# Performance work log

Measured on AMD Instinct MI355X. Metric: run time of the kernel, lower is better.

The kernel has to match this reference:

```python
import jax, jax.numpy as jnp
import numpy as np

B, N, D, H = 4, 1024, 1024, 16
DK = D // H
NEG_INF = jnp.finfo(jnp.float32).min


def setup_inputs() -> dict:
    key = jax.random.key(0)
    ks = jax.random.split(key, 6)
    x = jax.random.normal(ks[0], (B, N, D), dtype=jnp.float32)
    # padding mask: True where padded; vary lengths per batch element
    lengths = jnp.array([N, N - 128, N - 256, N - 512], dtype=jnp.int32)
    mask = jnp.arange(N)[None, :] >= lengths[:, None]  # [B, N] bool
    s = (1.0 / np.sqrt(D)).astype(np.float32)  # xavier-ish scale
    Wq = jax.random.normal(ks[1], (D, D), dtype=jnp.float32) * s
    Wk = jax.random.normal(ks[2], (D, D), dtype=jnp.float32) * s
    Wv = jax.random.normal(ks[3], (D, D), dtype=jnp.float32) * s
    Wo = jax.random.normal(ks[4], (D, D), dtype=jnp.float32) * s
    z = jnp.zeros((D,), dtype=jnp.float32)
    return {"x": x, "mask": mask, "Wq": Wq, "bq": z, "Wk": Wk, "bk": z,
            "Wv": Wv, "bv": z, "Wo": Wo, "bo": z}


def reference(x, mask, Wq, bq, Wk, bk, Wv, bv, Wo, bo):
    b, n, d = x.shape
    scale = jnp.asarray(DK, x.dtype) ** -0.5
    # QKV projections (weights stored [out, in] like torch Linear)
    def proj(W, bias):
        y = jnp.einsum('bnd,ed->bne', x, W) + bias
        return y.reshape(b, n, H, DK).transpose(0, 2, 1, 3)  # [B,H,N,Dk]
    q = proj(Wq, bq)
    k = proj(Wk, bk)
    v = proj(Wv, bv)
    energy = jnp.einsum('bhqd,bhkd->bhqk', q, k) * scale  # [B,H,N,N]
    energy = jnp.where(mask[:, None, None, :], NEG_INF, energy)
    weights = jax.nn.softmax(energy, axis=-1)
    attn = jnp.einsum('bhqk,bhkd->bhqd', weights, v)  # [B,H,N,Dk]
    attn = attn.transpose(0, 2, 1, 3).reshape(b, n, d)
    return jnp.einsum('bnd,ed->bne', attn, Wo) + bo
```

## Files before the change

kernel.cpp:

```cpp
#include <hip/hip_runtime.h>

#define DEV __device__ __forceinline__

typedef __attribute__((ext_vector_type(8))) short s16x8;
typedef __attribute__((ext_vector_type(4))) float f32x4;
typedef __attribute__((ext_vector_type(4))) unsigned short u16x4;
typedef __attribute__((ext_vector_type(2))) unsigned int u32x2;

static constexpr int Bb = 4, Nn = 1024, Dd = 1024, Hh = 16, DKk = 64;

DEV unsigned short f2bf(float f) {
    union { float f; unsigned int u; } x; x.f = f;
    unsigned int r = x.u + 0x7FFFu + ((x.u >> 16) & 1u);
    return (unsigned short)(r >> 16);
}

DEV float fexp2(float x) {
#if __has_builtin(__builtin_amdgcn_exp2f)
    return __builtin_amdgcn_exp2f(x);
#else
    return exp2f(x);
#endif
}

DEV void gld16(const void* g, void* l) {
    __builtin_amdgcn_global_load_lds(
        (const __attribute__((address_space(1))) void*)g,
        (__attribute__((address_space(3))) void*)l, 16, 0, 0);
}

__global__ void decode_mask_k(const unsigned int* __restrict__ raw, int* __restrict__ lengths) {
    __shared__ int is_u8;
    const int tid = threadIdx.x;
    if (tid == 0) is_u8 = 0;
    __syncthreads();
    int nz = 0;
    for (int i = tid; i < 1024; i += 256) nz |= (raw[i] != 0u) ? 1 : 0;
    if (nz) is_u8 = 1;
    __syncthreads();
    const int wv = tid >> 6, lane = tid & 63;
    int cnt = 0;
    if (is_u8) {
        const unsigned char* b8 = (const unsigned char*)raw;
        for (int n = lane; n < Nn; n += 64) cnt += (b8[wv * Nn + n] == 0) ? 1 : 0;
    } else {
        for (int n = lane; n < Nn; n += 64) cnt += (raw[wv * Nn + n] == 0u) ? 1 : 0;
    }
#pragma unroll
    for (int off = 32; off; off >>= 1) cnt += __shfl_xor(cnt, off);
    if (lane == 0) lengths[wv] = cnt;
}

__global__ __launch_bounds__(256) void cast_k(const float* __restrict__ x,
                                              const float* __restrict__ Wq,
                                              const float* __restrict__ Wk,
                                              const float* __restrict__ Wv,
                                              const float* __restrict__ Wo,
                                              unsigned short* __restrict__ xb,
                                              unsigned short* __restrict__ Wqb,
                                              unsigned short* __restrict__ Wkb,
                                              unsigned short* __restrict__ Wvb,
                                              unsigned short* __restrict__ Wob) {
    const size_t i = ((size_t)blockIdx.x * 256 + threadIdx.x) * 8;
    const float* src;
    unsigned short* dst;
    size_t off;
    const size_t XE = (size_t)4 * 1024 * 1024, WE = (size_t)1024 * 1024;
    if (i < XE) {
        src = x; dst = xb; off = i;
    } else {
        size_t j = i - XE;
        int w = (int)(j >> 20);
        off = j & (WE - 1);
        src = (w == 0) ? Wq : (w == 1) ? Wk : (w == 2) ? Wv : Wo;
        dst = (w == 0) ? Wqb : (w == 1) ? Wkb : (w == 2) ? Wvb : Wob;
    }
    f32x4 a = *(const f32x4*)(src + off);
    f32x4 b = *(const f32x4*)(src + off + 4);
    s16x8 t;
    t[0] = (short)f2bf(a[0]); t[1] = (short)f2bf(a[1]);
    t[2] = (short)f2bf(a[2]); t[3] = (short)f2bf(a[3]);
    t[4] = (short)f2bf(b[0]); t[5] = (short)f2bf(b[1]);
    t[6] = (short)f2bf(b[2]); t[7] = (short)f2bf(b[3]);
    *(s16x8*)(dst + off) = t;
}

DEV void gemm_kloop(const unsigned short* __restrict__ A,
                    const unsigned short* __restrict__ W,
                    char* lA, char* lB, int bm, int bn,
                    int tid, int kstep0, f32x4 (&acc)[4][4]) {
    const int wv = tid >> 6, lane = tid & 63, g = lane >> 4, lr = lane & 15;
    const int wr = wv >> 1, wc = wv & 1;

    const int rbase = wv * 8 + (lane >> 3);
    const int corig = (lane & 7) ^ (lane >> 3);
    const unsigned short* Asrc = A + (size_t)(bm + rbase) * Dd + corig * 8;
    const unsigned short* Bsrc = W + (size_t)(bn + rbase) * Dd + corig * 8;
    const int ldsb = wv * 1024;
    const int xk = (lr & 7);

    int kstep = kstep0;
    for (int it = 0; it < 16; ++it) {
        const int k0 = kstep * 64;
#pragma unroll
        for (int p = 0; p < 4; ++p) {
            gld16(Asrc + (size_t)(p * 32) * Dd + k0, lA + p * 4096 + ldsb);
            gld16(Bsrc + (size_t)(p * 32) * Dd + k0, lB + p * 4096 + ldsb);
        }
        __syncthreads();
#pragma unroll
        for (int s = 0; s < 2; ++s) {
            s16x8 af[4], bf[4];
#pragma unroll
            for (int m = 0; m < 4; ++m)
                af[m] = *(const s16x8*)(lA + (wr * 64 + m * 16 + lr) * 128 + (((s * 4 + g) ^ xk) << 4));
#pragma unroll
            for (int n = 0; n < 4; ++n)
                bf[n] = *(const s16x8*)(lB + (wc * 64 + n * 16 + lr) * 128 + (((s * 4 + g) ^ xk) << 4));
#pragma unroll
            for (int m = 0; m < 4; ++m)
#pragma unroll
                for (int n = 0; n < 4; ++n)
                    acc[m][n] = __builtin_amdgcn_mfma_f32_16x16x32_bf16(af[m], bf[n], acc[m][n], 0, 0, 0);
        }
        __syncthreads();
        kstep = (kstep + 1) & 15;
    }
}

__global__ __launch_bounds__(256, 4) void gemm_qkv_k(const unsigned short* __restrict__ xb,
                                                     const unsigned short* __restrict__ Wqb,
                                                     const unsigned short* __restrict__ Wkb,
                                                     const unsigned short* __restrict__ Wvb,
                                                     const float* __restrict__ bq,
                                                     const float* __restrict__ bk,
                                                     const float* __restrict__ bv,
                                                     unsigned short* __restrict__ Qo,
                                                     unsigned short* __restrict__ Ko,
                                                     unsigned short* __restrict__ Vo) {
    __shared__ __align__(16) char lA[128 * 64 * 2];
    __shared__ __align__(16) char lB[128 * 64 * 2];
    const int z = blockIdx.z;
    const unsigned short* W = (z == 0) ? Wqb : (z == 1) ? Wkb : Wvb;
    const float* bias = (z == 0) ? bq : (z == 1) ? bk : bv;

    const int tid = threadIdx.x;
    const int wv = tid >> 6, lane = tid & 63, g = lane >> 4, lr = lane & 15;
    const int wr = wv >> 1, wc = wv & 1;
    const int bm = blockIdx.x * 128, bn = blockIdx.y * 128;
    const int kstep0 = (blockIdx.x * 5 + blockIdx.y * 3 + z * 7) & 15;

    f32x4 acc[4][4];
#pragma unroll
    for (int m = 0; m < 4; ++m)
#pragma unroll
        for (int n = 0; n < 4; ++n) acc[m][n] = (f32x4){0.f, 0.f, 0.f, 0.f};

    gemm_kloop(xb, W, lA, lB, bm, bn, tid, kstep0, acc);

    const int row0 = bm + wr * 64 + g * 4;
    if (z == 0) {
        const float qs = 0.125f * 1.44269504f;
#pragma unroll
        for (int m = 0; m < 4; ++m)
#pragma unroll
            for (int n = 0; n < 4; ++n) {
                const int col = bn + wc * 64 + n * 16 + lr;
                const float bv_ = bias[col];
#pragma unroll
                for (int r = 0; r < 4; ++r)
                    Qo[(size_t)(row0 + m * 16 + r) * Dd + col] = f2bf((acc[m][n][r] + bv_) * qs);
            }
    } else if (z == 1) {
#pragma unroll
        for (int m = 0; m < 4; ++m)
#pragma unroll
            for (int n = 0; n < 4; ++n) {
                const int col = bn + wc * 64 + n * 16 + lr;
                const int h = col >> 6, dk = col & 63;
                const float bv_ = bias[col];
#pragma unroll
                for (int r = 0; r < 4; ++r) {
                    const int rowg = row0 + m * 16 + r;
                    const int b_ = rowg >> 10, tok = rowg & 1023;
                    size_t idx = ((size_t)(b_ * Hh + h) * Nn + tok) * DKk +
                                 (((dk >> 3) ^ (tok & 7)) << 3) + (dk & 7);
                    Ko[idx] = f2bf(acc[m][n][r] + bv_);
                }
            }
    } else {
#pragma unroll
        for (int m = 0; m < 4; ++m)
#pragma unroll
            for (int n = 0; n < 4; ++n) {
                const int col = bn + wc * 64 + n * 16 + lr;
                const int h = col >> 6, dk = col & 63;
                const float bv_ = bias[col];
                const int rowg = row0 + m * 16;
                const int b_ = rowg >> 10, tok = rowg & 1023;
                u16x4 t;
#pragma unroll
                for (int r = 0; r < 4; ++r) t[r] = f2bf(acc[m][n][r] + bv_);
                size_t idx = ((size_t)(b_ * Hh + h) * DKk + dk) * Nn + (tok & ~63) +
                             ((((tok >> 3) & 7) ^ (dk & 7)) << 3) + (tok & 7);
                *(u16x4*)(Vo + idx) = t;
            }
    }
}

__global__ __launch_bounds__(256, 4) void gemm_out_k(const unsigned short* __restrict__ Ab,
                                                     const unsigned short* __restrict__ Wob,
                                                     const float* __restrict__ bo,
                                                     float* __restrict__ out) {
    __shared__ __align__(16) char lA[128 * 64 * 2];
    __shared__ __align__(16) char lB[128 * 64 * 2];
    const int tid = threadIdx.x;
    const int wv = tid >> 6, lane = tid & 63, g = lane >> 4, lr = lane & 15;
    const int wr = wv >> 1, wc = wv & 1;
    const int bm = blockIdx.x * 128, bn = blockIdx.y * 128;
    const int kstep0 = (blockIdx.x * 5 + blockIdx.y * 3) & 15;

    f32x4 acc[4][4];
#pragma unroll
    for (int m = 0; m < 4; ++m)
#pragma unroll
        for (int n = 0; n < 4; ++n) acc[m][n] = (f32x4){0.f, 0.f, 0.f, 0.f};

    gemm_kloop(Ab, Wob, lA, lB, bm, bn, tid, kstep0, acc);

    const int row0 = bm + wr * 64 + g * 4;
#pragma unroll
    for (int m = 0; m < 4; ++m)
#pragma unroll
        for (int n = 0; n < 4; ++n) {
            const int col = bn + wc * 64 + n * 16 + lr;
            const float bv_ = bo[col];
#pragma unroll
            for (int r = 0; r < 4; ++r)
                out[(size_t)(row0 + m * 16 + r) * Dd + col] = acc[m][n][r] + bv_;
        }
}

__global__ __launch_bounds__(256) void attn_k(const unsigned short* __restrict__ Q,
                                              const unsigned short* __restrict__ Kg,
                                              const unsigned short* __restrict__ Vtg,
                                              const int* __restrict__ lengths,
                                              unsigned short* __restrict__ O) {
    const int tid = threadIdx.x;
    const int wv = tid >> 6, lane = tid & 63, g = lane >> 4, lr = lane & 15;
    const int bid = blockIdx.x;
    const int qt = bid & 15, h = (bid >> 4) & 15, b = bid >> 8;
    const int len = lengths[b];
    const int nt = (len + 63) >> 6;

    __shared__ __align__(16) char Ks[2 * 64 * 128];
    __shared__ __align__(16) char Vs[2 * 64 * 128];
    __shared__ __align__(16) char Ps[4][16 * 128];

    s16x8 qf[2];
    {
        const int qrow = b * Nn + qt * 64 + wv * 16 + lr;
        const unsigned short* qp = Q + (size_t)qrow * Dd + h * DKk + g * 8;
        qf[0] = *(const s16x8*)qp;
        qf[1] = *(const s16x8*)(qp + 32);
    }

    float m_run = -INFINITY, l_run = 0.f;
    f32x4 oacc[4];
#pragma unroll
    for (int dt = 0; dt < 4; ++dt) oacc[dt] = (f32x4){0.f, 0.f, 0.f, 0.f};

    const int s0 = wv * 64 + lane;
    const int r0 = s0 >> 3, c0 = s0 & 7;
    const int r1 = r0 + 32;
    const unsigned short* Kbase = Kg + (size_t)(b * Hh + h) * Nn * DKk;
    const unsigned short* Vbase = Vtg + (size_t)(b * Hh + h) * DKk * Nn;

    const int xk16 = (lr & 7) << 4;
    const int shsrc = (lane & 48) | (g * 4);

    {
        gld16(Kbase + (size_t)(0 + r0) * DKk + c0 * 8, Ks + wv * 1024);
        gld16(Kbase + (size_t)(0 + r1) * DKk + c0 * 8, Ks + wv * 1024 + 4096);
        gld16(Vbase + (size_t)r0 * Nn + 0 + c0 * 8, Vs + wv * 1024);
        gld16(Vbase + (size_t)r1 * Nn + 0 + c0 * 8, Vs + wv * 1024 + 4096);
    }
    __syncthreads();

    int cur = 0;
    for (int kt = 0; kt < nt; ++kt) {
        const int kb = kt * 64;
        if (kt + 1 < nt) {
            const int nb = (cur ^ 1) * 8192, kb2 = kb + 64;
            gld16(Kbase + (size_t)(kb2 + r0) * DKk + c0 * 8, Ks + nb + wv * 1024);
            gld16(Kbase + (size_t)(kb2 + r1) * DKk + c0 * 8, Ks + nb + wv * 1024 + 4096);
            gld16(Vbase + (size_t)r0 * Nn + kb2 + c0 * 8, Vs + nb + wv * 1024);
            gld16(Vbase + (size_t)r1 * Nn + kb2 + c0 * 8, Vs + nb + wv * 1024 + 4096);
        }
        const char* ks_ = Ks + cur * 8192;
        const char* vs_ = Vs + cur * 8192;

        f32x4 sfr[4];
        __builtin_amdgcn_s_setprio(1);
#pragma unroll
        for (int ct = 0; ct < 4; ++ct) {
            f32x4 c = (f32x4){0.f, 0.f, 0.f, 0.f};
#pragma unroll
            for (int s = 0; s < 2; ++s) {
                s16x8 kf = *(const s16x8*)(ks_ + (ct * 16 + lr) * 128 + ((((s * 4 + g) << 4)) ^ xk16));
                c = __builtin_amdgcn_mfma_f32_16x16x32_bf16(kf, qf[s], c, 0, 0, 0);
            }
            sfr[ct] = c;
        }
        __builtin_amdgcn_s_setprio(0);

        float mx = -INFINITY;
        if (kb + 64 <= len) {
#pragma unroll
            for (int ct = 0; ct < 4; ++ct)
#pragma unroll
                for (int r = 0; r < 4; ++r) mx = fmaxf(mx, sfr[ct][r]);
        } else {
#pragma unroll
            for (int ct = 0; ct < 4; ++ct) {
                const int kb4 = kb + ct * 16 + g * 4;
#pragma unroll
                for (int r = 0; r < 4; ++r) {
                    const float s_ = (kb4 + r < len) ? sfr[ct][r] : -INFINITY;
                    sfr[ct][r] = s_;
                    mx = fmaxf(mx, s_);
                }
            }
        }
        mx = fmaxf(mx, __shfl_xor(mx, 16));
        mx = fmaxf(mx, __shfl_xor(mx, 32));

        if (__any(mx > m_run + 8.f)) {
            const float mn = fmaxf(m_run, mx);
            const float alpha = fexp2(m_run - mn);
            m_run = mn;
            l_run *= alpha;
            float ao[4];
#pragma unroll
            for (int r = 0; r < 4; ++r) ao[r] = __shfl(alpha, shsrc + r);
#pragma unroll
            for (int dt = 0; dt < 4; ++dt)
#pragma unroll
                for (int r = 0; r < 4; ++r) oacc[dt][r] *= ao[r];
        }

        float ls = 0.f;
#pragma unroll
        for (int ct = 0; ct < 4; ++ct)
#pragma unroll
            for (int r = 0; r < 4; ++r) {
                const float p = fexp2(sfr[ct][r] - m_run);
                sfr[ct][r] = p;
                ls += p;
            }
        ls += __shfl_xor(ls, 16);
        ls += __shfl_xor(ls, 32);
        l_run += ls;

#pragma unroll
        for (int ct = 0; ct < 4; ++ct) {
            unsigned int w0, w1;
            asm("v_cvt_pk_bf16_f32 %0, %1, %2" : "=v"(w0) : "v"(sfr[ct][0]), "v"(sfr[ct][1]));
            asm("v_cvt_pk_bf16_f32 %0, %1, %2" : "=v"(w1) : "v"(sfr[ct][2]), "v"(sfr[ct][3]));
            u32x2 wp; wp[0] = w0; wp[1] = w1;
            *(u32x2*)(Ps[wv] + lr * 128 + ((ct * 32 + g * 8) ^ xk16)) = wp;
        }

        __builtin_amdgcn_s_setprio(1);
#pragma unroll
        for (int s = 0; s < 2; ++s) {
            s16x8 pf = *(const s16x8*)(Ps[wv] + lr * 128 + ((((s * 4 + g) << 4)) ^ xk16));
#pragma unroll
            for (int dt = 0; dt < 4; ++dt) {
                s16x8 vf = *(const s16x8*)(vs_ + (dt * 16 + lr) * 128 + ((((s * 4 + g) << 4)) ^ xk16));
                oacc[dt] = __builtin_amdgcn_mfma_f32_16x16x32_bf16(pf, vf, oacc[dt], 0, 0, 0);
            }
        }
        __builtin_amdgcn_s_setprio(0);
        __syncthreads();
        cur ^= 1;
    }

    float lo[4];
#pragma unroll
    for (int r = 0; r < 4; ++r) lo[r] = __shfl(l_run, shsrc + r);
#pragma unroll
    for (int dt = 0; dt < 4; ++dt) {
        const int col = h * DKk + dt * 16 + lr;
#pragma unroll
        for (int r = 0; r < 4; ++r) {
            const int row = qt * 64 + wv * 16 + g * 4 + r;
            float v = oacc[dt][r] / lo[r];
            O[(size_t)(b * Nn + row) * Dd + col] = f2bf(v);
        }
    }
}

extern "C" void kernel_launch(void* const* d_in, const int* in_sizes, int n_in,
                              void* d_out, int out_size, void* d_ws, size_t ws_size,
                              hipStream_t stream) {
    const float* x  = (const float*)d_in[0];
    const unsigned int* mraw = (const unsigned int*)d_in[1];
    const float* Wq = (const float*)d_in[2];
    const float* bq = (const float*)d_in[3];
    const float* Wk = (const float*)d_in[4];
    const float* bk = (const float*)d_in[5];
    const float* Wv = (const float*)d_in[6];
    const float* bv = (const float*)d_in[7];
    const float* Wo = (const float*)d_in[8];
    const float* bo = (const float*)d_in[9];

    char* ws = (char*)d_ws;
    int* lengths        = (int*)ws;                      ws += 1 << 16;
    unsigned short* xb  = (unsigned short*)ws;           ws += (size_t)Bb * Nn * Dd * 2;
    unsigned short* Wqb = (unsigned short*)ws;           ws += (size_t)Dd * Dd * 2;
    unsigned short* Wkb = (unsigned short*)ws;           ws += (size_t)Dd * Dd * 2;
    unsigned short* Wvb = (unsigned short*)ws;           ws += (size_t)Dd * Dd * 2;
    unsigned short* Wob = (unsigned short*)ws;           ws += (size_t)Dd * Dd * 2;
    unsigned short* Qb  = (unsigned short*)ws;           ws += (size_t)Bb * Nn * Dd * 2;
    unsigned short* Kg  = (unsigned short*)ws;           ws += (size_t)Bb * Nn * Dd * 2;
    unsigned short* Vtg = (unsigned short*)ws;           ws += (size_t)Bb * Nn * Dd * 2;
    unsigned short* Ab  = (unsigned short*)ws;

    decode_mask_k<<<1, 256, 0, stream>>>(mraw, lengths);
    cast_k<<<4096, 256, 0, stream>>>(x, Wq, Wk, Wv, Wo, xb, Wqb, Wkb, Wvb, Wob);

    dim3 qkv_grid(Bb * Nn / 128, Dd / 128, 3);
    gemm_qkv_k<<<qkv_grid, 256, 0, stream>>>(xb, Wqb, Wkb, Wvb, bq, bk, bv, Qb, Kg, Vtg);

    attn_k<<<Bb * Hh * (Nn / 64), 256, 0, stream>>>(Qb, Kg, Vtg, lengths, Ab);

    dim3 out_grid(Bb * Nn / 128, Dd / 128);
    gemm_out_k<<<out_grid, 256, 0, stream>>>(Ab, Wob, bo, (float*)d_out);
}
```

Baseline: 96.40 us.

## Double-buffer GEMM k-loop and attention loads with partial vmcnt waits

The GEMM k-loop moves from single-buffered 64-wide K steps with full syncs to double-buffered 32-wide steps. The next tile's global-to-LDS loads are issued before computing the current tile, and the wait is vmcnt(4) followed by a raw s_barrier. The LDS layout changes to a k-major, unswizzled arrangement. The attention kernel drops its full syncthreads in favour of the same partial wait, always issuing a (dummy on the last step) prefetch so the vmcnt count stays constant. The aim is to overlap memory latency with MFMA work; the risks are LDS bank conflicts from the unswizzled layout and correctness depending on the ordering of the raw barriers.

```diff
diff --git a/kernel.cpp b/kernel.cpp
--- a/kernel.cpp
+++ b/kernel.cpp
@@ -27,6 +27,13 @@
     __builtin_amdgcn_global_load_lds(
         (const __attribute__((address_space(1))) void*)g,
         (__attribute__((address_space(3))) void*)l, 16, 0, 0);
+}
+
+DEV void wait_vm4_barrier() {
+    __builtin_amdgcn_sched_barrier(0);
+    asm volatile("s_waitcnt vmcnt(4)" ::: "memory");
+    __builtin_amdgcn_sched_barrier(0);
+    __builtin_amdgcn_s_barrier();
 }
 
 __global__ void decode_mask_k(const unsigned int* __restrict__ raw, int* __restrict__ lengths) {
@@ -92,39 +99,49 @@
     const int wv = tid >> 6, lane = tid & 63, g = lane >> 4, lr = lane & 15;
     const int wr = wv >> 1, wc = wv & 1;
 
-    const int rbase = wv * 8 + (lane >> 3);
-    const int corig = (lane & 7) ^ (lane >> 3);
-    const unsigned short* Asrc = A + (size_t)(bm + rbase) * Dd + corig * 8;
-    const unsigned short* Bsrc = W + (size_t)(bn + rbase) * Dd + corig * 8;
-    const int ldsb = wv * 1024;
-    const int xk = (lr & 7);
+    const unsigned short* Asrc = A + (size_t)(bm + (tid & 127)) * Dd + (tid >> 7) * 8;
+    const unsigned short* Bsrc = W + (size_t)(bn + (tid & 127)) * Dd + (tid >> 7) * 8;
+    const int ldsb0 = wv * 1024;
+    const int ldsb1 = wv * 1024 + 4096;
 
     int kstep = kstep0;
-    for (int it = 0; it < 16; ++it) {
-        const int k0 = kstep * 64;
-#pragma unroll
-        for (int p = 0; p < 4; ++p) {
-            gld16(Asrc + (size_t)(p * 32) * Dd + k0, lA + p * 4096 + ldsb);
-            gld16(Bsrc + (size_t)(p * 32) * Dd + k0, lB + p * 4096 + ldsb);
-        }
-        __syncthreads();
-#pragma unroll
-        for (int s = 0; s < 2; ++s) {
-            s16x8 af[4], bf[4];
-#pragma unroll
-            for (int m = 0; m < 4; ++m)
-                af[m] = *(const s16x8*)(lA + (wr * 64 + m * 16 + lr) * 128 + (((s * 4 + g) ^ xk) << 4));
+    {
+        const int k0 = kstep * 32;
+        gld16(Asrc + k0, lA + ldsb0);
+        gld16(Asrc + k0 + 16, lA + ldsb1);
+        gld16(Bsrc + k0, lB + ldsb0);
+        gld16(Bsrc + k0 + 16, lB + ldsb1);
+    }
+    int cur = 0;
+    for (int it = 0; it < 32; ++it) {
+        const int knext = (kstep + 1) & 31;
+        const int k1 = knext * 32, nb = (cur ^ 1) * 8192;
+        gld16(Asrc + k1, lA + nb + ldsb0);
+        gld16(Asrc + k1 + 16, lA + nb + ldsb1);
+        gld16(Bsrc + k1, lB + nb + ldsb0);
+        gld16(Bsrc + k1 + 16, lB + nb + ldsb1);
+
+        wait_vm4_barrier();
+
+        const char* a_ = lA + cur * 8192;
+        const char* b_ = lB + cur * 8192;
+        s16x8 af[4], bf[4];
+#pragma unroll
+        for (int m = 0; m < 4; ++m)
+            af[m] = *(const s16x8*)(a_ + (g * 128 + wr * 64 + m * 16 + lr) * 16);
+#pragma unroll
+        for (int n = 0; n < 4; ++n)
+            bf[n] = *(const s16x8*)(b_ + (g * 128 + wc * 64 + n * 16 + lr) * 16);
+        __builtin_amdgcn_s_setprio(1);
+#pragma unroll
+        for (int m = 0; m < 4; ++m)
 #pragma unroll
             for (int n = 0; n < 4; ++n)
-                bf[n] = *(const s16x8*)(lB + (wc * 64 + n * 16 + lr) * 128 + (((s * 4 + g) ^ xk) << 4));
-#pragma unroll
-            for (int m = 0; m < 4; ++m)
-#pragma unroll
-                for (int n = 0; n < 4; ++n)
-                    acc[m][n] = __builtin_amdgcn_mfma_f32_16x16x32_bf16(af[m], bf[n], acc[m][n], 0, 0, 0);
-        }
-        __syncthreads();
-        kstep = (kstep + 1) & 15;
+                acc[m][n] = __builtin_amdgcn_mfma_f32_16x16x32_bf16(af[m], bf[n], acc[m][n], 0, 0, 0);
+        __builtin_amdgcn_s_setprio(0);
+        __builtin_amdgcn_s_barrier();
+        cur ^= 1;
+        kstep = knext;
     }
 }
 
@@ -138,8 +155,8 @@
                                                      unsigned short* __restrict__ Qo,
                                                      unsigned short* __restrict__ Ko,
                                                      unsigned short* __restrict__ Vo) {
-    __shared__ __align__(16) char lA[128 * 64 * 2];
-    __shared__ __align__(16) char lB[128 * 64 * 2];
+    __shared__ __align__(16) char lA[2 * 128 * 32 * 2];
+    __shared__ __align__(16) char lB[2 * 128 * 32 * 2];
     const int z = blockIdx.z;
     const unsigned short* W = (z == 0) ? Wqb : (z == 1) ? Wkb : Wvb;
     const float* bias = (z == 0) ? bq : (z == 1) ? bk : bv;
@@ -148,7 +165,7 @@
     const int wv = tid >> 6, lane = tid & 63, g = lane >> 4, lr = lane & 15;
     const int wr = wv >> 1, wc = wv & 1;
     const int bm = blockIdx.x * 128, bn = blockIdx.y * 128;
-    const int kstep0 = (blockIdx.x * 5 + blockIdx.y * 3 + z * 7) & 15;
+    const int kstep0 = (blockIdx.x * 5 + blockIdx.y * 3 + z * 7) & 31;
 
     f32x4 acc[4][4];
 #pragma unroll
@@ -212,13 +229,13 @@
                                                      const unsigned short* __restrict__ Wob,
                                                      const float* __restrict__ bo,
                                                      float* __restrict__ out) {
-    __shared__ __align__(16) char lA[128 * 64 * 2];
-    __shared__ __align__(16) char lB[128 * 64 * 2];
+    __shared__ __align__(16) char lA[2 * 128 * 32 * 2];
+    __shared__ __align__(16) char lB[2 * 128 * 32 * 2];
     const int tid = threadIdx.x;
     const int wv = tid >> 6, lane = tid & 63, g = lane >> 4, lr = lane & 15;
     const int wr = wv >> 1, wc = wv & 1;
     const int bm = blockIdx.x * 128, bn = blockIdx.y * 128;
-    const int kstep0 = (blockIdx.x * 5 + blockIdx.y * 3) & 15;
+    const int kstep0 = (blockIdx.x * 5 + blockIdx.y * 3) & 31;
 
     f32x4 acc[4][4];
 #pragma unroll
@@ -279,24 +296,24 @@
     const int xk16 = (lr & 7) << 4;
     const int shsrc = (lane & 48) | (g * 4);
 
-    {
-        gld16(Kbase + (size_t)(0 + r0) * DKk + c0 * 8, Ks + wv * 1024);
-        gld16(Kbase + (size_t)(0 + r1) * DKk + c0 * 8, Ks + wv * 1024 + 4096);
-        gld16(Vbase + (size_t)r0 * Nn + 0 + c0 * 8, Vs + wv * 1024);
-        gld16(Vbase + (size_t)r1 * Nn + 0 + c0 * 8, Vs + wv * 1024 + 4096);
-    }
-    __syncthreads();
+    gld16(Kbase + (size_t)r0 * DKk + c0 * 8, Ks + wv * 1024);
+    gld16(Kbase + (size_t)r1 * DKk + c0 * 8, Ks + wv * 1024 + 4096);
+    gld16(Vbase + (size_t)r0 * Nn + c0 * 8, Vs + wv * 1024);
+    gld16(Vbase + (size_t)r1 * Nn + c0 * 8, Vs + wv * 1024 + 4096);
 
     int cur = 0;
     for (int kt = 0; kt < nt; ++kt) {
         const int kb = kt * 64;
-        if (kt + 1 < nt) {
-            const int nb = (cur ^ 1) * 8192, kb2 = kb + 64;
+        {
+            const int kb2 = (kt + 1 < nt) ? kb + 64 : 0;
+            const int nb = (cur ^ 1) * 8192;
             gld16(Kbase + (size_t)(kb2 + r0) * DKk + c0 * 8, Ks + nb + wv * 1024);
             gld16(Kbase + (size_t)(kb2 + r1) * DKk + c0 * 8, Ks + nb + wv * 1024 + 4096);
             gld16(Vbase + (size_t)r0 * Nn + kb2 + c0 * 8, Vs + nb + wv * 1024);
             gld16(Vbase + (size_t)r1 * Nn + kb2 + c0 * 8, Vs + nb + wv * 1024 + 4096);
         }
+        wait_vm4_barrier();
+
         const char* ks_ = Ks + cur * 8192;
         const char* vs_ = Vs + cur * 8192;
 
@@ -382,7 +399,7 @@
             }
         }
         __builtin_amdgcn_s_setprio(0);
-        __syncthreads();
+        __builtin_amdgcn_s_barrier();
         cur ^= 1;
     }
 
```

Result: slower. 140.4 us (+45.7%).

## Double-buffer GEMM LDS tiles and use partial vmcnt waits for prefetch overlap

Applied to the files above, without the earlier changes.

The GEMM k-loop now double-buffers its A/B LDS tiles, issuing the next k-step's global-to-LDS loads before computing on the current buffer. A partial s_waitcnt vmcnt(8) followed by a barrier waits only for the older loads, so fetches overlap MFMA work. The attention loop likewise switches from __syncthreads to vmcnt(4)+barrier, always issuing a (possibly dummy) prefetch so the count stays uniform. MFMA sections get raised priority. The cost is doubled GEMM LDS, with launch bounds lowered from 4 to 2 blocks per SM, plus reliance on hand-counted vmcnt values, and the last iterations load redundant tiles.

```diff
diff --git a/kernel.cpp b/kernel.cpp
--- a/kernel.cpp
+++ b/kernel.cpp
@@ -27,6 +27,19 @@
     __builtin_amdgcn_global_load_lds(
         (const __attribute__((address_space(1))) void*)g,
         (__attribute__((address_space(3))) void*)l, 16, 0, 0);
+}
+
+DEV void wait_vm4_barrier() {
+    __builtin_amdgcn_sched_barrier(0);
+    asm volatile("s_waitcnt vmcnt(4)" ::: "memory");
+    __builtin_amdgcn_sched_barrier(0);
+    __builtin_amdgcn_s_barrier();
+}
+DEV void wait_vm8_barrier() {
+    __builtin_amdgcn_sched_barrier(0);
+    asm volatile("s_waitcnt vmcnt(8)" ::: "memory");
+    __builtin_amdgcn_sched_barrier(0);
+    __builtin_amdgcn_s_barrier();
 }
 
 __global__ void decode_mask_k(const unsigned int* __restrict__ raw, int* __restrict__ lengths) {
@@ -100,35 +113,52 @@
     const int xk = (lr & 7);
 
     int kstep = kstep0;
-    for (int it = 0; it < 16; ++it) {
+    {
         const int k0 = kstep * 64;
 #pragma unroll
         for (int p = 0; p < 4; ++p) {
             gld16(Asrc + (size_t)(p * 32) * Dd + k0, lA + p * 4096 + ldsb);
             gld16(Bsrc + (size_t)(p * 32) * Dd + k0, lB + p * 4096 + ldsb);
         }
-        __syncthreads();
+    }
+    int cur = 0;
+    for (int it = 0; it < 16; ++it) {
+        const int knext = (kstep + 1) & 15;
+        const int k1 = knext * 64, nb = (cur ^ 1) * 16384;
+#pragma unroll
+        for (int p = 0; p < 4; ++p) {
+            gld16(Asrc + (size_t)(p * 32) * Dd + k1, lA + nb + p * 4096 + ldsb);
+            gld16(Bsrc + (size_t)(p * 32) * Dd + k1, lB + nb + p * 4096 + ldsb);
+        }
+
+        wait_vm8_barrier();
+
+        const char* a_ = lA + cur * 16384;
+        const char* b_ = lB + cur * 16384;
 #pragma unroll
         for (int s = 0; s < 2; ++s) {
             s16x8 af[4], bf[4];
 #pragma unroll
             for (int m = 0; m < 4; ++m)
-                af[m] = *(const s16x8*)(lA + (wr * 64 + m * 16 + lr) * 128 + (((s * 4 + g) ^ xk) << 4));
+                af[m] = *(const s16x8*)(a_ + (wr * 64 + m * 16 + lr) * 128 + (((s * 4 + g) ^ xk) << 4));
 #pragma unroll
             for (int n = 0; n < 4; ++n)
-                bf[n] = *(const s16x8*)(lB + (wc * 64 + n * 16 + lr) * 128 + (((s * 4 + g) ^ xk) << 4));
+                bf[n] = *(const s16x8*)(b_ + (wc * 64 + n * 16 + lr) * 128 + (((s * 4 + g) ^ xk) << 4));
+            __builtin_amdgcn_s_setprio(1);
 #pragma unroll
             for (int m = 0; m < 4; ++m)
 #pragma unroll
                 for (int n = 0; n < 4; ++n)
                     acc[m][n] = __builtin_amdgcn_mfma_f32_16x16x32_bf16(af[m], bf[n], acc[m][n], 0, 0, 0);
-        }
-        __syncthreads();
-        kstep = (kstep + 1) & 15;
-    }
-}
-
-__global__ __launch_bounds__(256, 4) void gemm_qkv_k(const unsigned short* __restrict__ xb,
+            __builtin_amdgcn_s_setprio(0);
+        }
+        __builtin_amdgcn_s_barrier();
+        cur ^= 1;
+        kstep = knext;
+    }
+}
+
+__global__ __launch_bounds__(256, 2) void gemm_qkv_k(const unsigned short* __restrict__ xb,
                                                      const unsigned short* __restrict__ Wqb,
                                                      const unsigned short* __restrict__ Wkb,
                                                      const unsigned short* __restrict__ Wvb,
@@ -138,8 +168,8 @@
                                                      unsigned short* __restrict__ Qo,
                                                      unsigned short* __restrict__ Ko,
                                                      unsigned short* __restrict__ Vo) {
-    __shared__ __align__(16) char lA[128 * 64 * 2];
-    __shared__ __align__(16) char lB[128 * 64 * 2];
+    __shared__ __align__(16) char lA[2 * 128 * 64 * 2];
+    __shared__ __align__(16) char lB[2 * 128 * 64 * 2];
     const int z = blockIdx.z;
     const unsigned short* W = (z == 0) ? Wqb : (z == 1) ? Wkb : Wvb;
     const float* bias = (z == 0) ? bq : (z == 1) ? bk : bv;
@@ -208,12 +238,12 @@
     }
 }
 
-__global__ __launch_bounds__(256, 4) void gemm_out_k(const unsigned short* __restrict__ Ab,
+__global__ __launch_bounds__(256, 2) void gemm_out_k(const unsigned short* __restrict__ Ab,
                                                      const unsigned short* __restrict__ Wob,
                                                      const float* __restrict__ bo,
                                                      float* __restrict__ out) {
-    __shared__ __align__(16) char lA[128 * 64 * 2];
-    __shared__ __align__(16) char lB[128 * 64 * 2];
+    __shared__ __align__(16) char lA[2 * 128 * 64 * 2];
+    __shared__ __align__(16) char lB[2 * 128 * 64 * 2];
     const int tid = threadIdx.x;
     const int wv = tid >> 6, lane = tid & 63, g = lane >> 4, lr = lane & 15;
     const int wr = wv >> 1, wc = wv & 1;
@@ -279,24 +309,24 @@
     const int xk16 = (lr & 7) << 4;
     const int shsrc = (lane & 48) | (g * 4);
 
-    {
-        gld16(Kbase + (size_t)(0 + r0) * DKk + c0 * 8, Ks + wv * 1024);
-        gld16(Kbase + (size_t)(0 + r1) * DKk + c0 * 8, Ks + wv * 1024 + 4096);
-        gld16(Vbase + (size_t)r0 * Nn + 0 + c0 * 8, Vs + wv * 1024);
-        gld16(Vbase + (size_t)r1 * Nn + 0 + c0 * 8, Vs + wv * 1024 + 4096);
-    }
-    __syncthreads();
+    gld16(Kbase + (size_t)r0 * DKk + c0 * 8, Ks + wv * 1024);
+    gld16(Kbase + (size_t)r1 * DKk + c0 * 8, Ks + wv * 1024 + 4096);
+    gld16(Vbase + (size_t)r0 * Nn + c0 * 8, Vs + wv * 1024);
+    gld16(Vbase + (size_t)r1 * Nn + c0 * 8, Vs + wv * 1024 + 4096);
 
     int cur = 0;
     for (int kt = 0; kt < nt; ++kt) {
         const int kb = kt * 64;
-        if (kt + 1 < nt) {
-            const int nb = (cur ^ 1) * 8192, kb2 = kb + 64;
+        {
+            const int kb2 = (kt + 1 < nt) ? kb + 64 : 0;
+            const int nb = (cur ^ 1) * 8192;
             gld16(Kbase + (size_t)(kb2 + r0) * DKk + c0 * 8, Ks + nb + wv * 1024);
             gld16(Kbase + (size_t)(kb2 + r1) * DKk + c0 * 8, Ks + nb + wv * 1024 + 4096);
             gld16(Vbase + (size_t)r0 * Nn + kb2 + c0 * 8, Vs + nb + wv * 1024);
             gld16(Vbase + (size_t)r1 * Nn + kb2 + c0 * 8, Vs + nb + wv * 1024 + 4096);
         }
+        wait_vm4_barrier();
+
         const char* ks_ = Ks + cur * 8192;
         const char* vs_ = Vs + cur * 8192;
 
@@ -382,7 +412,7 @@
             }
         }
         __builtin_amdgcn_s_setprio(0);
-        __syncthreads();
+        __builtin_amdgcn_s_barrier();
         cur ^= 1;
     }
 
```

Result: slower. 103.4 us (+7.3%).

## Fold mask decode into cast kernel and pipeline attention loads with vmcnt waits

Applied to the files above, without the earlier changes.

Merges the mask-length decode kernel into the cast kernel as an extra block, which removes one kernel launch. In the attention loop, the full __syncthreads after the prologue is replaced by a per-iteration s_waitcnt vmcnt(4) plus a raw barrier. A dummy prefetch is always issued so the wait count stays constant, letting the next tile's loads remain in flight while the current tile computes. The softmax running max is folded into the MFMA accumulator initialisation (bias by -m_run), which drops a subtract per element; the cost is extra redundant loads on the last tile and reliance on hand-counted vmcnt correctness.

```diff
diff --git a/kernel.cpp b/kernel.cpp
--- a/kernel.cpp
+++ b/kernel.cpp
@@ -29,26 +29,11 @@
         (__attribute__((address_space(3))) void*)l, 16, 0, 0);
 }
 
-__global__ void decode_mask_k(const unsigned int* __restrict__ raw, int* __restrict__ lengths) {
-    __shared__ int is_u8;
-    const int tid = threadIdx.x;
-    if (tid == 0) is_u8 = 0;
-    __syncthreads();
-    int nz = 0;
-    for (int i = tid; i < 1024; i += 256) nz |= (raw[i] != 0u) ? 1 : 0;
-    if (nz) is_u8 = 1;
-    __syncthreads();
-    const int wv = tid >> 6, lane = tid & 63;
-    int cnt = 0;
-    if (is_u8) {
-        const unsigned char* b8 = (const unsigned char*)raw;
-        for (int n = lane; n < Nn; n += 64) cnt += (b8[wv * Nn + n] == 0) ? 1 : 0;
-    } else {
-        for (int n = lane; n < Nn; n += 64) cnt += (raw[wv * Nn + n] == 0u) ? 1 : 0;
-    }
-#pragma unroll
-    for (int off = 32; off; off >>= 1) cnt += __shfl_xor(cnt, off);
-    if (lane == 0) lengths[wv] = cnt;
+DEV void wait_vm4_barrier() {
+    __builtin_amdgcn_sched_barrier(0);
+    asm volatile("s_waitcnt vmcnt(4)" ::: "memory");
+    __builtin_amdgcn_sched_barrier(0);
+    __builtin_amdgcn_s_barrier();
 }
 
 __global__ __launch_bounds__(256) void cast_k(const float* __restrict__ x,
@@ -56,11 +41,35 @@
                                               const float* __restrict__ Wk,
                                               const float* __restrict__ Wv,
                                               const float* __restrict__ Wo,
+                                              const unsigned int* __restrict__ mraw,
                                               unsigned short* __restrict__ xb,
                                               unsigned short* __restrict__ Wqb,
                                               unsigned short* __restrict__ Wkb,
                                               unsigned short* __restrict__ Wvb,
-                                              unsigned short* __restrict__ Wob) {
+                                              unsigned short* __restrict__ Wob,
+                                              int* __restrict__ lengths) {
+    if (blockIdx.x == 4096) {
+        __shared__ int is_u8;
+        const int tid = threadIdx.x;
+        if (tid == 0) is_u8 = 0;
+        __syncthreads();
+        int nz = 0;
+        for (int i = tid; i < 1024; i += 256) nz |= (mraw[i] != 0u) ? 1 : 0;
+        if (nz) is_u8 = 1;
+        __syncthreads();
+        const int wv = tid >> 6, lane = tid & 63;
+        int cnt = 0;
+        if (is_u8) {
+            const unsigned char* b8 = (const unsigned char*)mraw;
+            for (int n = lane; n < Nn; n += 64) cnt += (b8[wv * Nn + n] == 0) ? 1 : 0;
+        } else {
+            for (int n = lane; n < Nn; n += 64) cnt += (mraw[wv * Nn + n] == 0u) ? 1 : 0;
+        }
+#pragma unroll
+        for (int off = 32; off; off >>= 1) cnt += __shfl_xor(cnt, off);
+        if (lane == 0) lengths[wv] = cnt;
+        return;
+    }
     const size_t i = ((size_t)blockIdx.x * 256 + threadIdx.x) * 8;
     const float* src;
     unsigned short* dst;
@@ -265,7 +274,7 @@
         qf[1] = *(const s16x8*)(qp + 32);
     }
 
-    float m_run = -INFINITY, l_run = 0.f;
+    float m_run = 0.f, l_run = 0.f;
     f32x4 oacc[4];
 #pragma unroll
     for (int dt = 0; dt < 4; ++dt) oacc[dt] = (f32x4){0.f, 0.f, 0.f, 0.f};
@@ -279,32 +288,33 @@
     const int xk16 = (lr & 7) << 4;
     const int shsrc = (lane & 48) | (g * 4);
 
-    {
-        gld16(Kbase + (size_t)(0 + r0) * DKk + c0 * 8, Ks + wv * 1024);
-        gld16(Kbase + (size_t)(0 + r1) * DKk + c0 * 8, Ks + wv * 1024 + 4096);
-        gld16(Vbase + (size_t)r0 * Nn + 0 + c0 * 8, Vs + wv * 1024);
-        gld16(Vbase + (size_t)r1 * Nn + 0 + c0 * 8, Vs + wv * 1024 + 4096);
-    }
-    __syncthreads();
+    gld16(Kbase + (size_t)r0 * DKk + c0 * 8, Ks + wv * 1024);
+    gld16(Kbase + (size_t)r1 * DKk + c0 * 8, Ks + wv * 1024 + 4096);
+    gld16(Vbase + (size_t)r0 * Nn + c0 * 8, Vs + wv * 1024);
+    gld16(Vbase + (size_t)r1 * Nn + c0 * 8, Vs + wv * 1024 + 4096);
 
     int cur = 0;
     for (int kt = 0; kt < nt; ++kt) {
         const int kb = kt * 64;
-        if (kt + 1 < nt) {
-            const int nb = (cur ^ 1) * 8192, kb2 = kb + 64;
+        {
+            const int kb2 = (kt + 1 < nt) ? kb + 64 : 0;
+            const int nb = (cur ^ 1) * 8192;
             gld16(Kbase + (size_t)(kb2 + r0) * DKk + c0 * 8, Ks + nb + wv * 1024);
             gld16(Kbase + (size_t)(kb2 + r1) * DKk + c0 * 8, Ks + nb + wv * 1024 + 4096);
             gld16(Vbase + (size_t)r0 * Nn + kb2 + c0 * 8, Vs + nb + wv * 1024);
             gld16(Vbase + (size_t)r1 * Nn + kb2 + c0 * 8, Vs + nb + wv * 1024 + 4096);
         }
+        wait_vm4_barrier();
+
         const char* ks_ = Ks + cur * 8192;
         const char* vs_ = Vs + cur * 8192;
 
+        const float nm = -m_run;
         f32x4 sfr[4];
         __builtin_amdgcn_s_setprio(1);
 #pragma unroll
         for (int ct = 0; ct < 4; ++ct) {
-            f32x4 c = (f32x4){0.f, 0.f, 0.f, 0.f};
+            f32x4 c = (f32x4){nm, nm, nm, nm};
 #pragma unroll
             for (int s = 0; s < 2; ++s) {
                 s16x8 kf = *(const s16x8*)(ks_ + (ct * 16 + lr) * 128 + ((((s * 4 + g) << 4)) ^ xk16));
@@ -335,10 +345,11 @@
         mx = fmaxf(mx, __shfl_xor(mx, 16));
         mx = fmaxf(mx, __shfl_xor(mx, 32));
 
-        if (__any(mx > m_run + 8.f)) {
-            const float mn = fmaxf(m_run, mx);
-            const float alpha = fexp2(m_run - mn);
-            m_run = mn;
+        float ls = 0.f;
+        if (__any(mx > 8.f)) {
+            const float dm = fmaxf(mx, 0.f);
+            const float alpha = fexp2(-dm);
+            m_run += dm;
             l_run *= alpha;
             float ao[4];
 #pragma unroll
@@ -347,17 +358,24 @@
             for (int dt = 0; dt < 4; ++dt)
 #pragma unroll
                 for (int r = 0; r < 4; ++r) oacc[dt][r] *= ao[r];
-        }
-
-        float ls = 0.f;
-#pragma unroll
-        for (int ct = 0; ct < 4; ++ct)
-#pragma unroll
-            for (int r = 0; r < 4; ++r) {
-                const float p = fexp2(sfr[ct][r] - m_run);
-                sfr[ct][r] = p;
-                ls += p;
-            }
+#pragma unroll
+            for (int ct = 0; ct < 4; ++ct)
+#pragma unroll
+                for (int r = 0; r < 4; ++r) {
+                    const float p = fexp2(sfr[ct][r] - dm);
+                    sfr[ct][r] = p;
+                    ls += p;
+                }
+        } else {
+#pragma unroll
+            for (int ct = 0; ct < 4; ++ct)
+#pragma unroll
+                for (int r = 0; r < 4; ++r) {
+                    const float p = fexp2(sfr[ct][r]);
+                    sfr[ct][r] = p;
+                    ls += p;
+                }
+        }
         ls += __shfl_xor(ls, 16);
         ls += __shfl_xor(ls, 32);
         l_run += ls;
@@ -382,7 +400,7 @@
             }
         }
         __builtin_amdgcn_s_setprio(0);
-        __syncthreads();
+        __builtin_amdgcn_s_barrier();
         cur ^= 1;
     }
 
@@ -427,8 +445,8 @@
     unsigned short* Vtg = (unsigned short*)ws;           ws += (size_t)Bb * Nn * Dd * 2;
     unsigned short* Ab  = (unsigned short*)ws;
 
-    decode_mask_k<<<1, 256, 0, stream>>>(mraw, lengths);
-    cast_k<<<4096, 256, 0, stream>>>(x, Wq, Wk, Wv, Wo, xb, Wqb, Wkb, Wvb, Wob);
+    cast_k<<<4097, 256, 0, stream>>>(x, Wq, Wk, Wv, Wo, mraw,
+                                     xb, Wqb, Wkb, Wvb, Wob, lengths);
 
     dim3 qkv_grid(Bb * Nn / 128, Dd / 128, 3);
     gemm_qkv_k<<<qkv_grid, 256, 0, stream>>>(xb, Wqb, Wkb, Wvb, bq, bk, bv, Qb, Kg, Vtg);
```

Result: faster. 93.73 us (-2.8%).
